# Performance work log

Measured on AMD Instinct MI355X. Metric: run time of the kernel, lower is better.

## Reference

```python
import jax, jax.numpy as jnp
import numpy as np

# Graph sampling geometry (2-layer neighbor sampling, fanouts 16 and 10)
N0 = 1_048_576   # layer-0 src nodes (full frontier, features supplied)
N1 = 65_536      # layer-0 dst nodes == layer-1 src nodes
N2 = 4_096       # layer-1 dst nodes (seeds)
DEG0, DEG1 = 16, 10
E0, E1 = N1 * DEG0, N2 * DEG1
D_IN, D_H, D_OUT = 128, 256, 47


def _init_linear(key, out_f, in_f):
    s = 1.0 / np.sqrt(in_f)
    return jax.random.uniform(key, (out_f, in_f), jnp.float32, -s, s)


def setup_inputs() -> dict:
    key = jax.random.key(0)
    ks = jax.random.split(key, 10)
    x = jax.random.normal(ks[0], (N0, D_IN), dtype=jnp.float32)
    # CSC: indptr over dst nodes (uniform degree), indices = src node ids
    indptr0 = jnp.arange(N1 + 1, dtype=jnp.int32) * DEG0
    indices0 = jax.random.randint(ks[1], (E0,), 0, N0, dtype=jnp.int32)
    indptr1 = jnp.arange(N2 + 1, dtype=jnp.int32) * DEG1
    indices1 = jax.random.randint(ks[2], (E1,), 0, N1, dtype=jnp.int32)
    return {
        "x": x,
        "indices0": indices0, "indptr0": indptr0,
        "indices1": indices1, "indptr1": indptr1,
        "Wl0": _init_linear(ks[3], D_H, D_IN), "bl0": jnp.zeros((D_H,), jnp.float32),
        "Wr0": _init_linear(ks[4], D_H, D_IN),
        "Wl1": _init_linear(ks[5], D_H, D_H), "bl1": jnp.zeros((D_H,), jnp.float32),
        "Wr1": _init_linear(ks[6], D_H, D_H),
        "Wo": _init_linear(ks[7], D_OUT, D_H), "bo": jnp.zeros((D_OUT,), jnp.float32),
    }


def expand_indptr(indptr, num_edges):
    # gb.expand_indptr: edge e -> dst j with indptr[j] <= e < indptr[j+1]
    e = jnp.arange(num_edges, dtype=indptr.dtype)
    return jnp.searchsorted(indptr, e, side="right") - 1


def sage_conv(h, src, dst, dst_size, Wl, bl, Wr):
    # PyG SAGEConv (mean aggr): lin_l(mean_{neighbors}) + lin_r(x_dst)
    msg = h[src]                                                    # [E, d]
    summed = jax.ops.segment_sum(msg, dst, num_segments=dst_size)  # [dst, d]
    cnt = jax.ops.segment_sum(jnp.ones_like(dst, dtype=h.dtype), dst,
                              num_segments=dst_size)
    mean = summed / jnp.maximum(cnt, 1.0)[:, None]
    return mean @ Wl.T + bl + h[:dst_size] @ Wr.T


def reference(x, indices0, indptr0, indices1, indptr1,
              Wl0, bl0, Wr0, Wl1, bl1, Wr1, Wo, bo):
    # layer 0
    dst0 = expand_indptr(indptr0, E0)
    h = sage_conv(x, indices0, dst0, N1, Wl0, bl0, Wr0)
    h = jax.nn.gelu(h, approximate=False)  # dropout p=0.0 -> identity
    # layer 1
    dst1 = expand_indptr(indptr1, E1)
    h = sage_conv(h, indices1, dst1, N2, Wl1, bl1, Wr1)
    h = jax.nn.gelu(h, approximate=False)
    # final projection
    return h @ Wo.T + bo
```

## Files before the change

kernel.cpp:

```cpp
#include <hip/hip_runtime.h>
#include <math.h>

#define N0 1048576
#define N1 65536
#define N2 4096
#define DEG0 16
#define DEG1 10
#define D_IN 128
#define D_H 256
#define D_OUT 47

__device__ __forceinline__ float gelu_exact(float x) {
    return 0.5f * x * (1.0f + erff(x * 0.70710678118654752f));
}

template <int DEG, int F4>
__global__ __launch_bounds__(256) void agg_mean_kernel(
    const float4* __restrict__ feat, const int* __restrict__ idx,
    float4* __restrict__ out, int ndst)
{
    const int lane  = threadIdx.x % F4;
    const int local = threadIdx.x / F4;
    const int per_block = 256 / F4;
    const int j = blockIdx.x * per_block + local;
    if (j >= ndst) return;

    const int* ip = idx + (long)j * DEG;
    int srcs[DEG];
#pragma unroll
    for (int e = 0; e < DEG; ++e) srcs[e] = ip[e];

    float4 acc = make_float4(0.f, 0.f, 0.f, 0.f);
#pragma unroll
    for (int e = 0; e < DEG; ++e) {
        float4 v = feat[(long)srcs[e] * F4 + lane];
        acc.x += v.x; acc.y += v.y; acc.z += v.z; acc.w += v.w;
    }
    const float r = 1.0f / (float)DEG;
    acc.x *= r; acc.y *= r; acc.z *= r; acc.w *= r;
    out[(long)j * F4 + lane] = acc;
}

template <int K1, int K2>
__global__ __launch_bounds__(256) void gemm_gelu_kernel(
    const float* __restrict__ A1, const float* __restrict__ A2,
    const float* __restrict__ B1, const float* __restrict__ B2,
    const float* __restrict__ bias, float* __restrict__ C, int M)
{
    constexpr int BM = 128, BN = 64, BK = 32;
    __shared__ float As[BK][BM + 4];
    __shared__ float Bs[BK][BN + 4];

    const int tid = threadIdx.x;
    const int bm = blockIdx.x, bn = blockIdx.y;
    const int tx = tid & 15;
    const int ty = tid >> 4;
    const int r  = tid >> 3;
    const int c4 = (tid & 7) * 4;

    float acc[8][4];
#pragma unroll
    for (int i = 0; i < 8; ++i)
#pragma unroll
        for (int j = 0; j < 4; ++j) acc[i][j] = 0.f;

    constexpr int KT = (K1 + K2) / BK;
#pragma unroll 1
    for (int kt = 0; kt < KT; ++kt) {
        const int k0 = kt * BK;
        const float* Asrc; const float* Bsrc; int koff;
        if (k0 < K1) { Asrc = A1; Bsrc = B1; koff = k0; }
        else         { Asrc = A2; Bsrc = B2; koff = k0 - K1; }
        const int lda = (k0 < K1) ? K1 : K2;

#pragma unroll
        for (int rr = 0; rr < 4; ++rr) {
            const int row = r + rr * 32;
            float4 v = *(const float4*)(Asrc + (long)(bm * BM + row) * lda + koff + c4);
            As[c4 + 0][row] = v.x; As[c4 + 1][row] = v.y;
            As[c4 + 2][row] = v.z; As[c4 + 3][row] = v.w;
        }
#pragma unroll
        for (int nn = 0; nn < 2; ++nn) {
            const int n = r + nn * 32;
            float4 v = *(const float4*)(Bsrc + (long)(bn * BN + n) * lda + koff + c4);
            Bs[c4 + 0][n] = v.x; Bs[c4 + 1][n] = v.y;
            Bs[c4 + 2][n] = v.z; Bs[c4 + 3][n] = v.w;
        }
        __syncthreads();

#pragma unroll
        for (int k = 0; k < BK; ++k) {
            float4 a0 = *(const float4*)&As[k][ty * 8];
            float4 a1 = *(const float4*)&As[k][ty * 8 + 4];
            float4 b  = *(const float4*)&Bs[k][tx * 4];
            const float av[8] = {a0.x, a0.y, a0.z, a0.w, a1.x, a1.y, a1.z, a1.w};
            const float bv[4] = {b.x, b.y, b.z, b.w};
#pragma unroll
            for (int i = 0; i < 8; ++i)
#pragma unroll
                for (int j = 0; j < 4; ++j)
                    acc[i][j] += av[i] * bv[j];
        }
        __syncthreads();
    }

    float4 b4 = *(const float4*)(bias + bn * BN + tx * 4);
    const float bb[4] = {b4.x, b4.y, b4.z, b4.w};
#pragma unroll
    for (int i = 0; i < 8; ++i) {
        const int row = bm * BM + ty * 8 + i;
        float4 o;
        o.x = gelu_exact(acc[i][0] + bb[0]);
        o.y = gelu_exact(acc[i][1] + bb[1]);
        o.z = gelu_exact(acc[i][2] + bb[2]);
        o.w = gelu_exact(acc[i][3] + bb[3]);
        *(float4*)(C + (long)row * D_H + bn * BN + tx * 4) = o;
    }
}

__global__ __launch_bounds__(64) void proj_kernel(
    const float* __restrict__ H, const float* __restrict__ Wo,
    const float* __restrict__ bo, float* __restrict__ out)
{
    __shared__ float hrow[D_H];
    const int i = blockIdx.x;
    ((float4*)hrow)[threadIdx.x] = ((const float4*)(H + (long)i * D_H))[threadIdx.x];
    __syncthreads();
    const int n = threadIdx.x;
    if (n < D_OUT) {
        const float* w = Wo + (long)n * D_H;
        float s = 0.f;
#pragma unroll 8
        for (int k = 0; k < D_H; ++k) s += hrow[k] * w[k];
        out[(long)i * D_OUT + n] = s + bo[n];
    }
}

extern "C" void kernel_launch(void* const* d_in, const int* in_sizes, int n_in,
                              void* d_out, int out_size, void* d_ws, size_t ws_size,
                              hipStream_t stream)
{
    const float* x        = (const float*)d_in[0];
    const int*   indices0 = (const int*)d_in[1];
    const int*   indices1 = (const int*)d_in[3];
    const float* Wl0 = (const float*)d_in[5];
    const float* bl0 = (const float*)d_in[6];
    const float* Wr0 = (const float*)d_in[7];
    const float* Wl1 = (const float*)d_in[8];
    const float* bl1 = (const float*)d_in[9];
    const float* Wr1 = (const float*)d_in[10];
    const float* Wo  = (const float*)d_in[11];
    const float* bo  = (const float*)d_in[12];
    float* out = (float*)d_out;

    float* mean0 = (float*)d_ws;
    float* h0    = mean0 + (size_t)N1 * D_IN;
    float* mean1 = h0    + (size_t)N1 * D_H;
    float* h1    = mean1 + (size_t)N2 * D_H;

    agg_mean_kernel<DEG0, D_IN / 4><<<N1 / (256 / (D_IN / 4)), 256, 0, stream>>>(
        (const float4*)x, indices0, (float4*)mean0, N1);

    gemm_gelu_kernel<D_IN, D_IN><<<dim3(N1 / 128, D_H / 64), 256, 0, stream>>>(
        mean0, x, Wl0, Wr0, bl0, h0, N1);

    agg_mean_kernel<DEG1, D_H / 4><<<N2 / (256 / (D_H / 4)), 256, 0, stream>>>(
        (const float4*)h0, indices1, (float4*)mean1, N2);

    gemm_gelu_kernel<D_H, D_H><<<dim3(N2 / 128, D_H / 64), 256, 0, stream>>>(
        mean1, h0, Wl1, Wr1, bl1, h1, N2);

    proj_kernel<<<N2, 64, 0, stream>>>(h1, Wo, bo, out);
}
```

Before: 869.9 us.

## Replace FP32 SIMT GEMMs with split-bf16 three-pass MFMA GEMMs

```diff
diff --git a/kernel.cpp b/kernel.cpp
--- a/kernel.cpp
+++ b/kernel.cpp
@@ -10,19 +10,64 @@
 #define D_H 256
 #define D_OUT 47
 
+typedef unsigned int uint32;
+typedef __attribute__((ext_vector_type(8))) short bf16x8;
+typedef __attribute__((ext_vector_type(4))) float f32x4;
+
+__device__ __forceinline__ unsigned short f2b(float x) {
+    uint32 u = __float_as_uint(x);
+    return (unsigned short)((u + 0x7fffu + ((u >> 16) & 1u)) >> 16);
+}
+__device__ __forceinline__ float b2f(unsigned short h) {
+    return __uint_as_float(((uint32)h) << 16);
+}
 __device__ __forceinline__ float gelu_exact(float x) {
     return 0.5f * x * (1.0f + erff(x * 0.70710678118654752f));
 }
 
+__global__ __launch_bounds__(256) void split_f32_kernel(
+    const float4* __restrict__ src, ushort4* __restrict__ hi,
+    ushort4* __restrict__ lo, int n4)
+{
+    int i = blockIdx.x * 256 + threadIdx.x;
+    if (i >= n4) return;
+    float4 v = src[i];
+    ushort4 h, l;
+    h.x = f2b(v.x); l.x = f2b(v.x - b2f(h.x));
+    h.y = f2b(v.y); l.y = f2b(v.y - b2f(h.y));
+    h.z = f2b(v.z); l.z = f2b(v.z - b2f(h.z));
+    h.w = f2b(v.w); l.w = f2b(v.w - b2f(h.w));
+    hi[i] = h; lo[i] = l;
+}
+
+__global__ __launch_bounds__(256) void prep_wo_kernel(
+    const float4* __restrict__ Wo, const float* __restrict__ bo,
+    ushort4* __restrict__ wh, ushort4* __restrict__ wl, float* __restrict__ bo_pad)
+{
+    int i = blockIdx.x * 256 + threadIdx.x;
+    if (i < 64 * D_H / 4) {
+        int row = (i * 4) >> 8;
+        float4 v = make_float4(0.f, 0.f, 0.f, 0.f);
+        if (row < D_OUT) v = Wo[i];
+        ushort4 h, l;
+        h.x = f2b(v.x); l.x = f2b(v.x - b2f(h.x));
+        h.y = f2b(v.y); l.y = f2b(v.y - b2f(h.y));
+        h.z = f2b(v.z); l.z = f2b(v.z - b2f(h.z));
+        h.w = f2b(v.w); l.w = f2b(v.w - b2f(h.w));
+        wh[i] = h; wl[i] = l;
+    }
+    if (blockIdx.x == 0 && threadIdx.x < 64)
+        bo_pad[threadIdx.x] = (threadIdx.x < D_OUT) ? bo[threadIdx.x] : 0.f;
+}
+
 template <int DEG, int F4>
-__global__ __launch_bounds__(256) void agg_mean_kernel(
+__global__ __launch_bounds__(256) void agg_split_f32(
     const float4* __restrict__ feat, const int* __restrict__ idx,
-    float4* __restrict__ out, int ndst)
+    ushort4* __restrict__ oh, ushort4* __restrict__ ol, int ndst)
 {
     const int lane  = threadIdx.x % F4;
     const int local = threadIdx.x / F4;
-    const int per_block = 256 / F4;
-    const int j = blockIdx.x * per_block + local;
+    const int j = blockIdx.x * (256 / F4) + local;
     if (j >= ndst) return;
 
     const int* ip = idx + (long)j * DEG;
@@ -38,102 +83,150 @@
     }
     const float r = 1.0f / (float)DEG;
     acc.x *= r; acc.y *= r; acc.z *= r; acc.w *= r;
-    out[(long)j * F4 + lane] = acc;
-}
-
-template <int K1, int K2>
-__global__ __launch_bounds__(256) void gemm_gelu_kernel(
-    const float* __restrict__ A1, const float* __restrict__ A2,
-    const float* __restrict__ B1, const float* __restrict__ B2,
-    const float* __restrict__ bias, float* __restrict__ C, int M)
-{
-    constexpr int BM = 128, BN = 64, BK = 32;
-    __shared__ float As[BK][BM + 4];
-    __shared__ float Bs[BK][BN + 4];
-
-    const int tid = threadIdx.x;
-    const int bm = blockIdx.x, bn = blockIdx.y;
-    const int tx = tid & 15;
-    const int ty = tid >> 4;
-    const int r  = tid >> 3;
-    const int c4 = (tid & 7) * 4;
-
-    float acc[8][4];
-#pragma unroll
-    for (int i = 0; i < 8; ++i)
-#pragma unroll
-        for (int j = 0; j < 4; ++j) acc[i][j] = 0.f;
+    ushort4 h, l;
+    h.x = f2b(acc.x); l.x = f2b(acc.x - b2f(h.x));
+    h.y = f2b(acc.y); l.y = f2b(acc.y - b2f(h.y));
+    h.z = f2b(acc.z); l.z = f2b(acc.z - b2f(h.z));
+    h.w = f2b(acc.w); l.w = f2b(acc.w - b2f(h.w));
+    oh[(long)j * F4 + lane] = h;
+    ol[(long)j * F4 + lane] = l;
+}
+
+template <int DEG, int F4>
+__global__ __launch_bounds__(256) void agg_split_bf16(
+    const ushort4* __restrict__ fh, const ushort4* __restrict__ fl,
+    const int* __restrict__ idx,
+    ushort4* __restrict__ oh, ushort4* __restrict__ ol, int ndst)
+{
+    const int lane  = threadIdx.x % F4;
+    const int local = threadIdx.x / F4;
+    const int j = blockIdx.x * (256 / F4) + local;
+    if (j >= ndst) return;
+
+    const int* ip = idx + (long)j * DEG;
+    int srcs[DEG];
+#pragma unroll
+    for (int e = 0; e < DEG; ++e) srcs[e] = ip[e];
+
+    float4 acc = make_float4(0.f, 0.f, 0.f, 0.f);
+#pragma unroll
+    for (int e = 0; e < DEG; ++e) {
+        long o = (long)srcs[e] * F4 + lane;
+        ushort4 h = fh[o], l = fl[o];
+        acc.x += b2f(h.x) + b2f(l.x);
+        acc.y += b2f(h.y) + b2f(l.y);
+        acc.z += b2f(h.z) + b2f(l.z);
+        acc.w += b2f(h.w) + b2f(l.w);
+    }
+    const float r = 1.0f / (float)DEG;
+    acc.x *= r; acc.y *= r; acc.z *= r; acc.w *= r;
+    ushort4 h, l;
+    h.x = f2b(acc.x); l.x = f2b(acc.x - b2f(h.x));
+    h.y = f2b(acc.y); l.y = f2b(acc.y - b2f(h.y));
+    h.z = f2b(acc.z); l.z = f2b(acc.z - b2f(h.z));
+    h.w = f2b(acc.w); l.w = f2b(acc.w - b2f(h.w));
+    oh[(long)j * F4 + lane] = h;
+    ol[(long)j * F4 + lane] = l;
+}
+
+template <int K1, int K2, bool GELU, bool SPLIT_OUT>
+__global__ __launch_bounds__(256) void gemm_mfma(
+    const unsigned short* __restrict__ A1h, const unsigned short* __restrict__ A1l,
+    const unsigned short* __restrict__ A2h, const unsigned short* __restrict__ A2l,
+    const unsigned short* __restrict__ B1h, const unsigned short* __restrict__ B1l,
+    const unsigned short* __restrict__ B2h, const unsigned short* __restrict__ B2l,
+    const float* __restrict__ bias,
+    float* __restrict__ Cf, unsigned short* __restrict__ Ch, unsigned short* __restrict__ Cl,
+    int ldc, int ncols)
+{
+    constexpr int BK = 32, LDK = 40;
+    __shared__ unsigned short sA[2][128][LDK];
+    __shared__ unsigned short sB[2][64][LDK];
+
+    const int tid  = threadIdx.x;
+    const int bm   = blockIdx.x, bn = blockIdx.y;
+    const int w    = tid >> 6;
+    const int lane = tid & 63;
+    const int quad = lane >> 4;
+    const int l16  = lane & 15;
+
+    f32x4 acc[2][4];
+#pragma unroll
+    for (int mt = 0; mt < 2; ++mt)
+#pragma unroll
+        for (int nt = 0; nt < 4; ++nt) acc[mt][nt] = (f32x4)0.f;
 
     constexpr int KT = (K1 + K2) / BK;
-#pragma unroll 1
     for (int kt = 0; kt < KT; ++kt) {
         const int k0 = kt * BK;
-        const float* Asrc; const float* Bsrc; int koff;
-        if (k0 < K1) { Asrc = A1; Bsrc = B1; koff = k0; }
-        else         { Asrc = A2; Bsrc = B2; koff = k0 - K1; }
-        const int lda = (k0 < K1) ? K1 : K2;
-
-#pragma unroll
-        for (int rr = 0; rr < 4; ++rr) {
-            const int row = r + rr * 32;
-            float4 v = *(const float4*)(Asrc + (long)(bm * BM + row) * lda + koff + c4);
-            As[c4 + 0][row] = v.x; As[c4 + 1][row] = v.y;
-            As[c4 + 2][row] = v.z; As[c4 + 3][row] = v.w;
-        }
-#pragma unroll
-        for (int nn = 0; nn < 2; ++nn) {
-            const int n = r + nn * 32;
-            float4 v = *(const float4*)(Bsrc + (long)(bn * BN + n) * lda + koff + c4);
-            Bs[c4 + 0][n] = v.x; Bs[c4 + 1][n] = v.y;
-            Bs[c4 + 2][n] = v.z; Bs[c4 + 3][n] = v.w;
+        const unsigned short *Ah, *Al, *Bh, *Bl;
+        int ka, koff;
+        if (k0 < K1) { Ah = A1h; Al = A1l; Bh = B1h; Bl = B1l; ka = K1; koff = k0; }
+        else         { Ah = A2h; Al = A2l; Bh = B2h; Bl = B2l; ka = (K2 ? K2 : 1); koff = k0 - K1; }
+
+#pragma unroll
+        for (int rep = 0; rep < 2; ++rep) {
+            int task = tid + rep * 256;
+            int row = task >> 2, seg = task & 3;
+            size_t g = (size_t)(bm * 128 + row) * ka + koff + seg * 8;
+            *(uint4*)&sA[0][row][seg * 8] = *(const uint4*)(Ah + g);
+            *(uint4*)&sA[1][row][seg * 8] = *(const uint4*)(Al + g);
+        }
+        {
+            int row = tid >> 2, seg = tid & 3;
+            size_t g = (size_t)(bn * 64 + row) * ka + koff + seg * 8;
+            *(uint4*)&sB[0][row][seg * 8] = *(const uint4*)(Bh + g);
+            *(uint4*)&sB[1][row][seg * 8] = *(const uint4*)(Bl + g);
         }
         __syncthreads();
 
-#pragma unroll
-        for (int k = 0; k < BK; ++k) {
-            float4 a0 = *(const float4*)&As[k][ty * 8];
-            float4 a1 = *(const float4*)&As[k][ty * 8 + 4];
-            float4 b  = *(const float4*)&Bs[k][tx * 4];
-            const float av[8] = {a0.x, a0.y, a0.z, a0.w, a1.x, a1.y, a1.z, a1.w};
-            const float bv[4] = {b.x, b.y, b.z, b.w};
-#pragma unroll
-            for (int i = 0; i < 8; ++i)
-#pragma unroll
-                for (int j = 0; j < 4; ++j)
-                    acc[i][j] += av[i] * bv[j];
-        }
+        bf16x8 Afh[2], Afl[2], Bfh[4], Bfl[4];
+#pragma unroll
+        for (int mt = 0; mt < 2; ++mt) {
+            int r = w * 32 + mt * 16 + l16;
+            Afh[mt] = *(const bf16x8*)&sA[0][r][quad * 8];
+            Afl[mt] = *(const bf16x8*)&sA[1][r][quad * 8];
+        }
+#pragma unroll
+        for (int nt = 0; nt < 4; ++nt) {
+            int r = nt * 16 + l16;
+            Bfh[nt] = *(const bf16x8*)&sB[0][r][quad * 8];
+            Bfl[nt] = *(const bf16x8*)&sB[1][r][quad * 8];
+        }
+#pragma unroll
+        for (int mt = 0; mt < 2; ++mt)
+#pragma unroll
+            for (int nt = 0; nt < 4; ++nt) {
+                acc[mt][nt] = __builtin_amdgcn_mfma_f32_16x16x32_bf16(
+                    Afl[mt], Bfh[nt], acc[mt][nt], 0, 0, 0);
+                acc[mt][nt] = __builtin_amdgcn_mfma_f32_16x16x32_bf16(
+                    Afh[mt], Bfl[nt], acc[mt][nt], 0, 0, 0);
+                acc[mt][nt] = __builtin_amdgcn_mfma_f32_16x16x32_bf16(
+                    Afh[mt], Bfh[nt], acc[mt][nt], 0, 0, 0);
+            }
         __syncthreads();
     }
 
-    float4 b4 = *(const float4*)(bias + bn * BN + tx * 4);
-    const float bb[4] = {b4.x, b4.y, b4.z, b4.w};
-#pragma unroll
-    for (int i = 0; i < 8; ++i) {
-        const int row = bm * BM + ty * 8 + i;
-        float4 o;
-        o.x = gelu_exact(acc[i][0] + bb[0]);
-        o.y = gelu_exact(acc[i][1] + bb[1]);
-        o.z = gelu_exact(acc[i][2] + bb[2]);
-        o.w = gelu_exact(acc[i][3] + bb[3]);
-        *(float4*)(C + (long)row * D_H + bn * BN + tx * 4) = o;
-    }
-}
-
-__global__ __launch_bounds__(64) void proj_kernel(
-    const float* __restrict__ H, const float* __restrict__ Wo,
-    const float* __restrict__ bo, float* __restrict__ out)
-{
-    __shared__ float hrow[D_H];
-    const int i = blockIdx.x;
-    ((float4*)hrow)[threadIdx.x] = ((const float4*)(H + (long)i * D_H))[threadIdx.x];
-    __syncthreads();
-    const int n = threadIdx.x;
-    if (n < D_OUT) {
-        const float* w = Wo + (long)n * D_H;
-        float s = 0.f;
-#pragma unroll 8
-        for (int k = 0; k < D_H; ++k) s += hrow[k] * w[k];
-        out[(long)i * D_OUT + n] = s + bo[n];
+#pragma unroll
+    for (int mt = 0; mt < 2; ++mt) {
+        const int row0 = bm * 128 + w * 32 + mt * 16 + quad * 4;
+#pragma unroll
+        for (int nt = 0; nt < 4; ++nt) {
+            const int col = bn * 64 + nt * 16 + l16;
+            const float bb = bias[col];
+#pragma unroll
+            for (int r = 0; r < 4; ++r) {
+                float v = acc[mt][nt][r] + bb;
+                if (GELU) v = gelu_exact(v);
+                if (SPLIT_OUT) {
+                    unsigned short h = f2b(v);
+                    Ch[(size_t)(row0 + r) * ldc + col] = h;
+                    Cl[(size_t)(row0 + r) * ldc + col] = f2b(v - b2f(h));
+                } else {
+                    if (col < ncols) Cf[(size_t)(row0 + r) * ldc + col] = v;
+                }
+            }
+        }
     }
 }
 
@@ -154,22 +247,52 @@
     const float* bo  = (const float*)d_in[12];
     float* out = (float*)d_out;
 
-    float* mean0 = (float*)d_ws;
-    float* h0    = mean0 + (size_t)N1 * D_IN;
-    float* mean1 = h0    + (size_t)N1 * D_H;
-    float* h1    = mean1 + (size_t)N2 * D_H;
-
-    agg_mean_kernel<DEG0, D_IN / 4><<<N1 / (256 / (D_IN / 4)), 256, 0, stream>>>(
-        (const float4*)x, indices0, (float4*)mean0, N1);
-
-    gemm_gelu_kernel<D_IN, D_IN><<<dim3(N1 / 128, D_H / 64), 256, 0, stream>>>(
-        mean0, x, Wl0, Wr0, bl0, h0, N1);
-
-    agg_mean_kernel<DEG1, D_H / 4><<<N2 / (256 / (D_H / 4)), 256, 0, stream>>>(
-        (const float4*)h0, indices1, (float4*)mean1, N2);
-
-    gemm_gelu_kernel<D_H, D_H><<<dim3(N2 / 128, D_H / 64), 256, 0, stream>>>(
-        mean1, h0, Wl1, Wr1, bl1, h1, N2);
-
-    proj_kernel<<<N2, 64, 0, stream>>>(h1, Wo, bo, out);
-}
+    unsigned short* p = (unsigned short*)d_ws;
+    unsigned short* xh   = p; p += (size_t)N1 * D_IN;
+    unsigned short* xl   = p; p += (size_t)N1 * D_IN;
+    unsigned short* m0h  = p; p += (size_t)N1 * D_IN;
+    unsigned short* m0l  = p; p += (size_t)N1 * D_IN;
+    unsigned short* h0h  = p; p += (size_t)N1 * D_H;
+    unsigned short* h0l  = p; p += (size_t)N1 * D_H;
+    unsigned short* m1h  = p; p += (size_t)N2 * D_H;
+    unsigned short* m1l  = p; p += (size_t)N2 * D_H;
+    unsigned short* h1h  = p; p += (size_t)N2 * D_H;
+    unsigned short* h1l  = p; p += (size_t)N2 * D_H;
+    unsigned short* wl0h = p; p += 256 * 128;
+    unsigned short* wl0l = p; p += 256 * 128;
+    unsigned short* wr0h = p; p += 256 * 128;
+    unsigned short* wr0l = p; p += 256 * 128;
+    unsigned short* wl1h = p; p += 256 * 256;
+    unsigned short* wl1l = p; p += 256 * 256;
+    unsigned short* wr1h = p; p += 256 * 256;
+    unsigned short* wr1l = p; p += 256 * 256;
+    unsigned short* woh  = p; p += 64 * 256;
+    unsigned short* wol  = p; p += 64 * 256;
+    float* bo_pad = (float*)p;
+
+    split_f32_kernel<<<32, 256, 0, stream>>>((const float4*)Wl0, (ushort4*)wl0h, (ushort4*)wl0l, 256 * 128 / 4);
+    split_f32_kernel<<<32, 256, 0, stream>>>((const float4*)Wr0, (ushort4*)wr0h, (ushort4*)wr0l, 256 * 128 / 4);
+    split_f32_kernel<<<64, 256, 0, stream>>>((const float4*)Wl1, (ushort4*)wl1h, (ushort4*)wl1l, 256 * 256 / 4);
+    split_f32_kernel<<<64, 256, 0, stream>>>((const float4*)Wr1, (ushort4*)wr1h, (ushort4*)wr1l, 256 * 256 / 4);
+    prep_wo_kernel<<<16, 256, 0, stream>>>((const float4*)Wo, bo, (ushort4*)woh, (ushort4*)wol, bo_pad);
+    split_f32_kernel<<<(N1 * D_IN / 4 + 255) / 256, 256, 0, stream>>>(
+        (const float4*)x, (ushort4*)xh, (ushort4*)xl, N1 * D_IN / 4);
+
+    agg_split_f32<DEG0, D_IN / 4><<<N1 / (256 / (D_IN / 4)), 256, 0, stream>>>(
+        (const float4*)x, indices0, (ushort4*)m0h, (ushort4*)m0l, N1);
+
+    gemm_mfma<D_IN, D_IN, true, true><<<dim3(N1 / 128, D_H / 64), 256, 0, stream>>>(
+        m0h, m0l, xh, xl, wl0h, wl0l, wr0h, wr0l, bl0,
+        nullptr, h0h, h0l, D_H, D_H);
+
+    agg_split_bf16<DEG1, D_H / 4><<<N2 / (256 / (D_H / 4)), 256, 0, stream>>>(
+        (const ushort4*)h0h, (const ushort4*)h0l, indices1, (ushort4*)m1h, (ushort4*)m1l, N2);
+
+    gemm_mfma<D_H, D_H, true, true><<<dim3(N2 / 128, D_H / 64), 256, 0, stream>>>(
+        m1h, m1l, h0h, h0l, wl1h, wl1l, wr1h, wr1l, bl1,
+        nullptr, h1h, h1l, D_H, D_H);
+
+    gemm_mfma<D_H, 0, false, false><<<dim3(N2 / 128, 1), 256, 0, stream>>>(
+        h1h, h1l, h1h, h1l, woh, wol, woh, wol, bo_pad,
+        out, nullptr, nullptr, D_OUT, D_OUT);
+}
```

After: 809.9 us. 1.07x faster.
